# Kernel optimization log

Hardware: AMD Instinct MI355X
Metric: run time of the kernel (lower is better)

## Reference

```python
import jax, jax.numpy as jnp
import numpy as np

N_BLOCKS = 16
N_HEADS = 2
HEAD_DIM = 32
SCALE = HEAD_DIM ** (-0.5)


def setup_inputs() -> dict:
    key = jax.random.key(0)
    ks = jax.random.split(key, 5)
    b, s, d = 16, 4096, 1024
    nb, bd = N_BLOCKS, 1024 // N_BLOCKS  # block_dim = 64; emb per-block dim = 64
    w_std = 1.0 / np.sqrt(bd)
    inp = {
        'x': jax.random.normal(ks[0], (b, s, d), dtype=jnp.float32),
        'wq': jax.random.normal(ks[1], (nb, bd, bd), dtype=jnp.float32) * w_std,
        'bq': jnp.zeros((nb, bd), dtype=jnp.float32),
        'wk': jax.random.normal(ks[2], (nb, bd, bd), dtype=jnp.float32) * w_std,
        'bk': jnp.zeros((nb, bd), dtype=jnp.float32),
        'wv': jax.random.normal(ks[3], (nb, bd, bd), dtype=jnp.float32) * w_std,
        'bv': jnp.zeros((nb, bd), dtype=jnp.float32),
        'wf': jax.random.normal(ks[4], (nb, bd, bd), dtype=jnp.float32) * w_std,
        'bf': jnp.zeros((nb, bd), dtype=jnp.float32),
    }
    return inp


def _group_linear(x, w, b):
    # x: [B, S, G*I] -> per-block linear -> [B, S, G*O]
    B, S, _ = x.shape
    G, I, O = w.shape
    xg = x.reshape(B, S, G, I)
    y = jnp.einsum('bsgi,gio->bsgo', xg, w) + b
    return y.reshape(B, S, G * O)


def reference(x, wq, bq, wk, bk, wv, bv, wf, bf):
    B, S, D = x.shape
    nb, nh, hd = N_BLOCKS, N_HEADS, HEAD_DIM
    # grouped QKV projections -> [B, S, nb, nh, hd] -> heads before blocks
    q = _group_linear(x, wq, bq).reshape(B, S, nb, nh, hd).transpose(0, 1, 3, 2, 4) * SCALE
    k = _group_linear(x, wk, bk).reshape(B, S, nb, nh, hd).transpose(0, 1, 3, 2, 4)
    v = _group_linear(x, wv, bv).reshape(B, S, nb, nh, hd).transpose(0, 1, 3, 2, 4)
    # attention across blocks: score [B, S, nh, nb, nb]
    score = jnp.einsum('bshgd,bshfd->bshgf', q, k)
    score = jax.nn.softmax(score, axis=-1)
    out = jnp.einsum('bshgf,bshfd->bshgd', score, v)
    # back to [B, S, nb, nh, hd] then flatten
    out = out.transpose(0, 1, 3, 2, 4).reshape(B, S, nb * nh * hd)
    out = _group_linear(out, wf, bf)
    return out.reshape(B, S, D)
```

## Files before the change

### kernel.cpp

```cpp
#include <hip/hip_runtime.h>
#include <hip/hip_bf16.h>
#include <stdint.h>


typedef __attribute__((ext_vector_type(8))) short bf16x8;
typedef __attribute__((ext_vector_type(4))) float f32x4;

#define NTOK   65536
#define DM     1024
#define TT     16
#define QSCALE 0.17677669529663687f
#define LOG2E  1.4426950408889634f

static __device__ __forceinline__ unsigned short f2bf(float f) {
  unsigned int u = __float_as_uint(f);
  u += 0x7fffu + ((u >> 16) & 1u);
  return (unsigned short)(u >> 16);
}

static __device__ __forceinline__ unsigned int pk2(float a, float b) {
  return (unsigned int)f2bf(a) | ((unsigned int)f2bf(b) << 16);
}

static __device__ __forceinline__ bf16x8 pack8(float4 a, float4 b) {
  bf16x8 r;
  r[0] = (short)f2bf(a.x); r[1] = (short)f2bf(a.y);
  r[2] = (short)f2bf(a.z); r[3] = (short)f2bf(a.w);
  r[4] = (short)f2bf(b.x); r[5] = (short)f2bf(b.y);
  r[6] = (short)f2bf(b.z); r[7] = (short)f2bf(b.w);
  return r;
}

union FragCast { uint4 u4; bf16x8 v; uint2 u2[2]; unsigned int u[4]; };

__global__ void build_wfrag(const float* __restrict__ wq, const float* __restrict__ wk,
                            const float* __restrict__ wv, const float* __restrict__ wf,
                            uint4* __restrict__ wfrag) {
  int tid = blockIdx.x * 256 + threadIdx.x;
  if (tid >= 4 * 16 * 2 * 4 * 64) return;
  int lane =  tid        & 63;
  int nf   = (tid >> 6)  & 3;
  int kk   = (tid >> 8)  & 1;
  int g    = (tid >> 9)  & 15;
  int mat  =  tid >> 13;
  const float* w = (mat == 0) ? wq : (mat == 1) ? wk : (mat == 2) ? wv : wf;
  float sc = (mat == 0) ? QSCALE : 1.0f;
  int o  = nf * 16 + (lane & 15);
  int kb = kk * 32 + 8 * (lane >> 4);
  unsigned int packed[4];
#pragma unroll
  for (int jj = 0; jj < 4; ++jj) {
    unsigned short lo = f2bf(w[(g * 64 + kb + 2 * jj    ) * 64 + o] * sc);
    unsigned short hi = f2bf(w[(g * 64 + kb + 2 * jj + 1) * 64 + o] * sc);
    packed[jj] = (unsigned int)lo | ((unsigned int)hi << 16);
  }
  uint4 u; u.x = packed[0]; u.y = packed[1]; u.z = packed[2]; u.w = packed[3];
  wfrag[tid] = u;
}

#define PH1(h_) do {                                                          \
  _Pragma("unroll")                                                           \
  for (int gi = 0; gi < 2; ++gi) {                                            \
    const int g = 2 * w + gi;                                                 \
    _Pragma("unroll")                                                         \
    for (int mat = 0; mat < 2; ++mat) {       \
      const float* bp = mat ? bk : bq;                                        \
      const float bsc = mat ? 1.0f : QSCALE;                                  \
      unsigned short* dst = mat ? s_k : s_q;                                  \
      _Pragma("unroll")                                                       \
      for (int nf2 = 0; nf2 < 2; ++nf2) {                                     \
        const int nf = 2 * (h_) + nf2;                                        \
        float4 b4 = *(const float4*)&bp[g * 64 + nf * 16 + 4 * lq];           \
        f32x4 a1 = {b4.x * bsc, b4.y * bsc, b4.z * bsc, b4.w * bsc};          \
        _Pragma("unroll")                                                     \
        for (int kk = 0; kk < 2; ++kk) {                                      \
          FragCast fc;                                                        \
          fc.u4 = wfrag[(((mat * 16 + g) * 2 + kk) * 4 + nf) * 64 + lane];    \
          a1 = __builtin_amdgcn_mfma_f32_16x16x32_bf16(fc.v, afr[gi][kk], a1, 0, 0, 0); \
        }                                                                     \
             \
        uint2 w2; w2.x = pk2(a1[0], a1[1]); w2.y = pk2(a1[2], a1[3]);         \
        const int blk = (16 * (2 * nf2 + (lq >> 1)) + g) ^ (lr & 7);          \
        *(uint2*)&dst[lr * 512 + blk * 8 + 4 * (lq & 1)] = w2;                \
      }                                                                       \
    }                                                                         \
    _Pragma("unroll")                                                         \
    for (int nf2 = 0; nf2 < 2; ++nf2) {         \
      const int nf = 2 * (h_) + nf2;                                          \
      const float bias = bv[g * 64 + nf * 16 + lr];                           \
      f32x4 a1 = {bias, bias, bias, bias};                                    \
      _Pragma("unroll")                                                       \
      for (int kk = 0; kk < 2; ++kk) {                                        \
        FragCast fc;                                                          \
        fc.u4 = wfrag[(((2 * 16 + g) * 2 + kk) * 4 + nf) * 64 + lane];        \
        a1 = __builtin_amdgcn_mfma_f32_16x16x32_bf16(afr[gi][kk], fc.v, a1, 0, 0, 0); \
      }                                                                       \
                   \
      const int L = 16 * (g >> 2) + lr;                                       \
      const int jj = g & 3;                                                   \
      _Pragma("unroll")                                                       \
      for (int r = 0; r < 4; ++r)                                             \
        s_v[((4 * lq + r) * 2 + nf2) * 256 + L * 4 + jj] = f2bf(a1[r]);       \
    }                                                                         \
  }                                                                           \
} while (0)

#define PH2() do {                                                            \
  _Pragma("unroll")                                                           \
  for (int tt = 0; tt < 2; ++tt) {                                            \
    const int t = 2 * w + tt;                                                 \
    f32x4 zero = {0.f, 0.f, 0.f, 0.f};                                        \
    FragCast qa, ka;                                                          \
    const int blk = lane ^ (t & 7);                                           \
    qa.u4 = *(const uint4*)&s_q[t * 512 + blk * 8];                           \
    ka.u4 = *(const uint4*)&s_k[t * 512 + blk * 8];                           \
                  \
    f32x4 sc4 = __builtin_amdgcn_mfma_f32_16x16x32_bf16(ka.v, qa.v, zero, 0, 0, 0); \
    float m = fmaxf(fmaxf(sc4[0], sc4[1]), fmaxf(sc4[2], sc4[3]));            \
    m = fmaxf(m, __shfl_xor(m, 16));                                          \
    m = fmaxf(m, __shfl_xor(m, 32));                                          \
    float p0 = exp2f((sc4[0] - m) * LOG2E);                                   \
    float p1 = exp2f((sc4[1] - m) * LOG2E);                                   \
    float p2 = exp2f((sc4[2] - m) * LOG2E);                                   \
    float p3 = exp2f((sc4[3] - m) * LOG2E);                                   \
    float s = p0 + p1 + p2 + p3;                                              \
    s += __shfl_xor(s, 16);                                                   \
    s += __shfl_xor(s, 32);                                                   \
    const float inv = __fdividef(1.0f, s);                                    \
    FragCast pa;                      \
    pa.u[0] = pk2(p0 * inv, p1 * inv);                                        \
    pa.u[1] = pk2(p2 * inv, p3 * inv);                                        \
    pa.u[2] = 0; pa.u[3] = 0;                                                 \
    _Pragma("unroll")                                                         \
    for (int nf = 0; nf < 2; ++nf) {                                          \
      FragCast va;              \
      va.u2[0] = *(const uint2*)&s_v[(t * 2 + nf) * 256 + lane * 4];          \
      va.u[2] = 0; va.u[3] = 0;                                               \
      f32x4 o4 = __builtin_amdgcn_mfma_f32_16x16x32_bf16(va.v, pa.v, zero, 0, 0, 0); \
                                   \
      uint2 w2; w2.x = pk2(o4[0], o4[1]); w2.y = pk2(o4[2], o4[3]);           \
      const int ablk = (16 * (2 * nf + (lq >> 1)) + lr) ^ (t & 7);            \
      *(uint2*)&s_att[t * 512 + ablk * 8 + 4 * (lq & 1)] = w2;                \
    }                                                                         \
  }                                                                           \
} while (0)

#define PH3(h_) do {                                                          \
  _Pragma("unroll")                                                           \
  for (int gi = 0; gi < 2; ++gi) {                                            \
    const int g = 2 * w + gi;                                                 \
    FragCast aa;                        \
    const int blk = (16 * lq + g) ^ (lr & 7);                                 \
    aa.u4 = *(const uint4*)&s_att[lr * 512 + blk * 8];                        \
    _Pragma("unroll")                                                         \
    for (int nf = 0; nf < 4; ++nf) {                                          \
      FragCast fc;                                                            \
      fc.u4 = wfrag[(((3 * 16 + g) * 2 + (h_)) * 4 + nf) * 64 + lane];        \
      acc[gi][nf] = __builtin_amdgcn_mfma_f32_16x16x32_bf16(fc.v, aa.v, acc[gi][nf], 0, 0, 0); \
    }                                                                         \
  }                                                                           \
} while (0)

__global__ __launch_bounds__(512, 4)
void fused_gc(const float* __restrict__ x,
              const float* __restrict__ bq, const float* __restrict__ bk,
              const float* __restrict__ bv, const float* __restrict__ bfb,
              const uint4* __restrict__ wfrag,
              float* __restrict__ out) {
  __shared__ __align__(16) unsigned short s_q  [16 * 512];
  __shared__ __align__(16) unsigned short s_k  [16 * 512];
  __shared__ __align__(16) unsigned short s_att[16 * 512];
  __shared__ __align__(16) unsigned short s_v  [16 * 2 * 64 * 4];

  const int tid  = threadIdx.x;
  const int w    = tid >> 6;
  const int lane = tid & 63;
  const int lr   = lane & 15;
  const int lq   = lane >> 4;
  const long tok0 = (long)blockIdx.x * TT;

  bf16x8 afr[2][2];
  {
    const float* xr = x + (tok0 + lr) * DM;
#pragma unroll
    for (int gi = 0; gi < 2; ++gi) {
      const int g = 2 * w + gi;
#pragma unroll
      for (int kk = 0; kk < 2; ++kk) {
        const float* p = xr + g * 64 + kk * 32 + 8 * lq;
        afr[gi][kk] = pack8(*(const float4*)p, *(const float4*)(p + 4));
      }
    }
  }

  f32x4 acc[2][4];

  PH1(0);
  __syncthreads();
  PH2();
  __syncthreads();

#pragma unroll
  for (int gi = 0; gi < 2; ++gi) {
    const int g = 2 * w + gi;
#pragma unroll
    for (int nf = 0; nf < 4; ++nf) {
      float4 b4 = *(const float4*)&bfb[g * 64 + nf * 16 + 4 * lq];
      acc[gi][nf][0] = b4.x; acc[gi][nf][1] = b4.y;
      acc[gi][nf][2] = b4.z; acc[gi][nf][3] = b4.w;
    }
  }
  PH3(0);
  PH1(1);
  __syncthreads();
  PH2();
  __syncthreads();
  PH3(1);

#pragma unroll
  for (int gi = 0; gi < 2; ++gi) {
    const int g = 2 * w + gi;
#pragma unroll
    for (int nf = 0; nf < 4; ++nf) {
      float4 o4;
      o4.x = acc[gi][nf][0]; o4.y = acc[gi][nf][1];
      o4.z = acc[gi][nf][2]; o4.w = acc[gi][nf][3];
      *(float4*)&out[(tok0 + lr) * DM + g * 64 + nf * 16 + 4 * lq] = o4;
    }
  }
}

extern "C" void kernel_launch(void* const* d_in, const int* in_sizes, int n_in,
                              void* d_out, int out_size, void* d_ws, size_t ws_size,
                              hipStream_t stream) {
  const float* x   = (const float*)d_in[0];
  const float* wq  = (const float*)d_in[1];
  const float* bq_ = (const float*)d_in[2];
  const float* wk  = (const float*)d_in[3];
  const float* bk_ = (const float*)d_in[4];
  const float* wv  = (const float*)d_in[5];
  const float* bv_ = (const float*)d_in[6];
  const float* wf  = (const float*)d_in[7];
  const float* bf_ = (const float*)d_in[8];
  (void)in_sizes; (void)n_in; (void)out_size; (void)ws_size;

  uint4* wfrag = (uint4*)d_ws;

  build_wfrag<<<128, 256, 0, stream>>>(wq, wk, wv, wf, wfrag);
  fused_gc<<<NTOK / TT, 512, 0, stream>>>(x, bq_, bk_, bv_, bf_, wfrag,
                                          (float*)d_out);
}
```

Before: 234.7 us.

## Batch-prefetch weight fragments ahead of MFMAs and use LDS-only barriers

Loads all Q/K/V weight fragments for each half into registers up front, and prefetches the output-projection fragments before the barriers so global loads overlap the PH2 attention phase. Replaces __syncthreads with a barrier that waits only on LDS counters, so in-flight global loads are not drained at each sync. It also swaps the manual bf16 rounding for the HIP intrinsic. This raises register pressure (24+8 extra uint4 fragments), which at launch bounds of 512 threads and 4 blocks may cause spills.

```diff
diff --git a/kernel.cpp b/kernel.cpp
--- a/kernel.cpp
+++ b/kernel.cpp
@@ -12,10 +12,15 @@
 #define QSCALE 0.17677669529663687f
 #define LOG2E  1.4426950408889634f
 
+#define WG_BARRIER() do {                                   \
+  asm volatile("s_waitcnt lgkmcnt(0)" ::: "memory");        \
+  __builtin_amdgcn_s_barrier();                             \
+} while (0)
+
 static __device__ __forceinline__ unsigned short f2bf(float f) {
-  unsigned int u = __float_as_uint(f);
-  u += 0x7fffu + ((u >> 16) & 1u);
-  return (unsigned short)(u >> 16);
+  union { __hip_bfloat16 h; unsigned short s; } cv;
+  cv.h = __float2bfloat16(f);
+  return cv.s;
 }
 
 static __device__ __forceinline__ unsigned int pk2(float a, float b) {
@@ -59,14 +64,30 @@
 }
 
 #define PH1(h_) do {                                                          \
+  FragCast fq[8], fk[8], fv[8];                                               \
   _Pragma("unroll")                                                           \
   for (int gi = 0; gi < 2; ++gi) {                                            \
     const int g = 2 * w + gi;                                                 \
     _Pragma("unroll")                                                         \
-    for (int mat = 0; mat < 2; ++mat) {       \
-      const float* bp = mat ? bk : bq;                                        \
-      const float bsc = mat ? 1.0f : QSCALE;                                  \
-      unsigned short* dst = mat ? s_k : s_q;                                  \
+    for (int kk = 0; kk < 2; ++kk) {                                          \
+      _Pragma("unroll")                                                       \
+      for (int nf2 = 0; nf2 < 2; ++nf2) {                                     \
+        const int nf = 2 * (h_) + nf2;                                        \
+        const int ix = gi * 4 + kk * 2 + nf2;                                 \
+        fq[ix].u4 = wfrag[(((0 * 16 + g) * 2 + kk) * 4 + nf) * 64 + lane];    \
+        fk[ix].u4 = wfrag[(((1 * 16 + g) * 2 + kk) * 4 + nf) * 64 + lane];    \
+        fv[ix].u4 = wfrag[(((2 * 16 + g) * 2 + kk) * 4 + nf) * 64 + lane];    \
+      }                                                                       \
+    }                                                                         \
+  }                                                                           \
+  _Pragma("unroll")                                                           \
+  for (int mat = 0; mat < 2; ++mat) {         \
+    const float* bp = mat ? bk : bq;                                          \
+    const float bsc = mat ? 1.0f : QSCALE;                                    \
+    unsigned short* dst = mat ? s_k : s_q;                                    \
+    _Pragma("unroll")                                                         \
+    for (int gi = 0; gi < 2; ++gi) {                                          \
+      const int g = 2 * w + gi;                                               \
       _Pragma("unroll")                                                       \
       for (int nf2 = 0; nf2 < 2; ++nf2) {                                     \
         const int nf = 2 * (h_) + nf2;                                        \
@@ -74,9 +95,9 @@
         f32x4 a1 = {b4.x * bsc, b4.y * bsc, b4.z * bsc, b4.w * bsc};          \
         _Pragma("unroll")                                                     \
         for (int kk = 0; kk < 2; ++kk) {                                      \
-          FragCast fc;                                                        \
-          fc.u4 = wfrag[(((mat * 16 + g) * 2 + kk) * 4 + nf) * 64 + lane];    \
-          a1 = __builtin_amdgcn_mfma_f32_16x16x32_bf16(fc.v, afr[gi][kk], a1, 0, 0, 0); \
+          a1 = __builtin_amdgcn_mfma_f32_16x16x32_bf16(                       \
+              (mat ? fk : fq)[gi * 4 + kk * 2 + nf2].v, afr[gi][kk], a1,      \
+              0, 0, 0);                                                       \
         }                                                                     \
              \
         uint2 w2; w2.x = pk2(a1[0], a1[1]); w2.y = pk2(a1[2], a1[3]);         \
@@ -84,16 +105,19 @@
         *(uint2*)&dst[lr * 512 + blk * 8 + 4 * (lq & 1)] = w2;                \
       }                                                                       \
     }                                                                         \
-    _Pragma("unroll")                                                         \
-    for (int nf2 = 0; nf2 < 2; ++nf2) {         \
+  }                                                                           \
+  _Pragma("unroll")                                                           \
+  for (int gi = 0; gi < 2; ++gi) {              \
+    const int g = 2 * w + gi;                                                 \
+    _Pragma("unroll")                                                         \
+    for (int nf2 = 0; nf2 < 2; ++nf2) {                                       \
       const int nf = 2 * (h_) + nf2;                                          \
       const float bias = bv[g * 64 + nf * 16 + lr];                           \
       f32x4 a1 = {bias, bias, bias, bias};                                    \
       _Pragma("unroll")                                                       \
       for (int kk = 0; kk < 2; ++kk) {                                        \
-        FragCast fc;                                                          \
-        fc.u4 = wfrag[(((2 * 16 + g) * 2 + kk) * 4 + nf) * 64 + lane];        \
-        a1 = __builtin_amdgcn_mfma_f32_16x16x32_bf16(afr[gi][kk], fc.v, a1, 0, 0, 0); \
+        a1 = __builtin_amdgcn_mfma_f32_16x16x32_bf16(                         \
+            afr[gi][kk], fv[gi * 4 + kk * 2 + nf2].v, a1, 0, 0, 0);           \
       }                                                                       \
                    \
       const int L = 16 * (g >> 2) + lr;                                       \
@@ -102,6 +126,16 @@
       for (int r = 0; r < 4; ++r)                                             \
         s_v[((4 * lq + r) * 2 + nf2) * 256 + L * 4 + jj] = f2bf(a1[r]);       \
     }                                                                         \
+  }                                                                           \
+} while (0)
+
+#define LOADF(h_) do {                                                        \
+  _Pragma("unroll")                                                           \
+  for (int gi = 0; gi < 2; ++gi) {                                            \
+    const int g = 2 * w + gi;                                                 \
+    _Pragma("unroll")                                                         \
+    for (int nf = 0; nf < 4; ++nf)                                            \
+      ff[gi * 4 + nf].u4 = wfrag[(((3 * 16 + g) * 2 + (h_)) * 4 + nf) * 64 + lane]; \
   }                                                                           \
 } while (0)
 
@@ -145,7 +179,7 @@
   }                                                                           \
 } while (0)
 
-#define PH3(h_) do {                                                          \
+#define PH3() do {                                                            \
   _Pragma("unroll")                                                           \
   for (int gi = 0; gi < 2; ++gi) {                                            \
     const int g = 2 * w + gi;                                                 \
@@ -154,9 +188,8 @@
     aa.u4 = *(const uint4*)&s_att[lr * 512 + blk * 8];                        \
     _Pragma("unroll")                                                         \
     for (int nf = 0; nf < 4; ++nf) {                                          \
-      FragCast fc;                                                            \
-      fc.u4 = wfrag[(((3 * 16 + g) * 2 + (h_)) * 4 + nf) * 64 + lane];        \
-      acc[gi][nf] = __builtin_amdgcn_mfma_f32_16x16x32_bf16(fc.v, aa.v, acc[gi][nf], 0, 0, 0); \
+      acc[gi][nf] = __builtin_amdgcn_mfma_f32_16x16x32_bf16(                  \
+          ff[gi * 4 + nf].v, aa.v, acc[gi][nf], 0, 0, 0);                     \
     }                                                                         \
   }                                                                           \
 } while (0)
@@ -194,12 +227,10 @@
   }
 
   f32x4 acc[2][4];
+  FragCast ff[8];
 
   PH1(0);
-  __syncthreads();
-  PH2();
-  __syncthreads();
-
+  LOADF(0);
 #pragma unroll
   for (int gi = 0; gi < 2; ++gi) {
     const int g = 2 * w + gi;
@@ -210,12 +241,16 @@
       acc[gi][nf][2] = b4.z; acc[gi][nf][3] = b4.w;
     }
   }
-  PH3(0);
+  WG_BARRIER();
+  PH2();
+  WG_BARRIER();
+  PH3();
   PH1(1);
-  __syncthreads();
+  LOADF(1);
+  WG_BARRIER();
   PH2();
-  __syncthreads();
-  PH3(1);
+  WG_BARRIER();
+  PH3();
 
 #pragma unroll
   for (int gi = 0; gi < 2; ++gi) {
```

Result: slower. 334.7 us (+42.6%).

## Split final grouped projection into separate kernel via global attention buffer

Applied to the files above, without the earlier changes.

When the workspace is large enough, the fused kernel stops after attention and writes bf16 attention outputs to a global buffer in MFMA fragment layout. A second kernel then runs the final grouped linear from that buffer. This frees the s_att shared memory and the output accumulators in the first kernel, which may raise occupancy, at the cost of an extra 128MB global round trip. It also swaps the manual bf16 rounding for the library conversion and hoists weight fragment loads in the QKV phase.

```diff
diff --git a/kernel.cpp b/kernel.cpp
--- a/kernel.cpp
+++ b/kernel.cpp
@@ -13,9 +13,9 @@
 #define LOG2E  1.4426950408889634f
 
 static __device__ __forceinline__ unsigned short f2bf(float f) {
-  unsigned int u = __float_as_uint(f);
-  u += 0x7fffu + ((u >> 16) & 1u);
-  return (unsigned short)(u >> 16);
+  union { __hip_bfloat16 h; unsigned short s; } cv;
+  cv.h = __float2bfloat16(f);
+  return cv.s;
 }
 
 static __device__ __forceinline__ unsigned int pk2(float a, float b) {
@@ -37,7 +37,7 @@
                             const float* __restrict__ wv, const float* __restrict__ wf,
                             uint4* __restrict__ wfrag) {
   int tid = blockIdx.x * 256 + threadIdx.x;
-  if (tid >= 4 * 16 * 2 * 4 * 64) return;
+  if (tid >= 5 * 16 * 2 * 4 * 64) return;
   int lane =  tid        & 63;
   int nf   = (tid >> 6)  & 3;
   int kk   = (tid >> 8)  & 1;
@@ -45,67 +45,94 @@
   int mat  =  tid >> 13;
   const float* w = (mat == 0) ? wq : (mat == 1) ? wk : (mat == 2) ? wv : wf;
   float sc = (mat == 0) ? QSCALE : 1.0f;
-  int o  = nf * 16 + (lane & 15);
-  int kb = kk * 32 + 8 * (lane >> 4);
+  int o = nf * 16 + (lane & 15);
   unsigned int packed[4];
-#pragma unroll
-  for (int jj = 0; jj < 4; ++jj) {
-    unsigned short lo = f2bf(w[(g * 64 + kb + 2 * jj    ) * 64 + o] * sc);
-    unsigned short hi = f2bf(w[(g * 64 + kb + 2 * jj + 1) * 64 + o] * sc);
-    packed[jj] = (unsigned int)lo | ((unsigned int)hi << 16);
+  if (mat == 4) {
+#pragma unroll
+    for (int jj = 0; jj < 4; ++jj) {
+      int d0 = kk * 32 + ((jj >> 1) ? 16 : 0) + 4 * (lane >> 4) + 2 * (jj & 1);
+      unsigned short lo = f2bf(w[(g * 64 + d0    ) * 64 + o]);
+      unsigned short hi = f2bf(w[(g * 64 + d0 + 1) * 64 + o]);
+      packed[jj] = (unsigned int)lo | ((unsigned int)hi << 16);
+    }
+  } else {
+    int kb = kk * 32 + 8 * (lane >> 4);
+#pragma unroll
+    for (int jj = 0; jj < 4; ++jj) {
+      unsigned short lo = f2bf(w[(g * 64 + kb + 2 * jj    ) * 64 + o] * sc);
+      unsigned short hi = f2bf(w[(g * 64 + kb + 2 * jj + 1) * 64 + o] * sc);
+      packed[jj] = (unsigned int)lo | ((unsigned int)hi << 16);
+    }
   }
   uint4 u; u.x = packed[0]; u.y = packed[1]; u.z = packed[2]; u.w = packed[3];
   wfrag[tid] = u;
 }
 
-#define PH1(h_) do {                                                          \
+#define QK_ONE(g_, gi_, nf2_, h_, fwa_, fwb_, bp_, bsc_, dst_) do {           \
+  const int nf = 2 * (h_) + (nf2_);                                           \
+  float4 b4 = *(const float4*)&(bp_)[(g_) * 64 + nf * 16 + 4 * lq];           \
+  f32x4 a1 = {b4.x * (bsc_), b4.y * (bsc_), b4.z * (bsc_), b4.w * (bsc_)};    \
+  a1 = __builtin_amdgcn_mfma_f32_16x16x32_bf16((fwa_).v, afr[gi_][0], a1, 0, 0, 0); \
+  a1 = __builtin_amdgcn_mfma_f32_16x16x32_bf16((fwb_).v, afr[gi_][1], a1, 0, 0, 0); \
+          \
+  uint2 w2; w2.x = pk2(a1[0], a1[1]); w2.y = pk2(a1[2], a1[3]);               \
+  const int blk = (16 * (2 * (nf2_) + (lq >> 1)) + (g_)) ^ (lr & 7);          \
+  *(uint2*)&(dst_)[lr * 512 + blk * 8 + 4 * (lq & 1)] = w2;                   \
+} while (0)
+
+#define PH1_MAT(h_, mofs_, bp_, bsc_, dst_) do {                              \
   _Pragma("unroll")                                                           \
   for (int gi = 0; gi < 2; ++gi) {                                            \
     const int g = 2 * w + gi;                                                 \
-    _Pragma("unroll")                                                         \
-    for (int mat = 0; mat < 2; ++mat) {       \
-      const float* bp = mat ? bk : bq;                                        \
-      const float bsc = mat ? 1.0f : QSCALE;                                  \
-      unsigned short* dst = mat ? s_k : s_q;                                  \
-      _Pragma("unroll")                                                       \
-      for (int nf2 = 0; nf2 < 2; ++nf2) {                                     \
-        const int nf = 2 * (h_) + nf2;                                        \
-        float4 b4 = *(const float4*)&bp[g * 64 + nf * 16 + 4 * lq];           \
-        f32x4 a1 = {b4.x * bsc, b4.y * bsc, b4.z * bsc, b4.w * bsc};          \
-        _Pragma("unroll")                                                     \
-        for (int kk = 0; kk < 2; ++kk) {                                      \
-          FragCast fc;                                                        \
-          fc.u4 = wfrag[(((mat * 16 + g) * 2 + kk) * 4 + nf) * 64 + lane];    \
-          a1 = __builtin_amdgcn_mfma_f32_16x16x32_bf16(fc.v, afr[gi][kk], a1, 0, 0, 0); \
-        }                                                                     \
-             \
-        uint2 w2; w2.x = pk2(a1[0], a1[1]); w2.y = pk2(a1[2], a1[3]);         \
-        const int blk = (16 * (2 * nf2 + (lq >> 1)) + g) ^ (lr & 7);          \
-        *(uint2*)&dst[lr * 512 + blk * 8 + 4 * (lq & 1)] = w2;                \
-      }                                                                       \
-    }                                                                         \
-    _Pragma("unroll")                                                         \
-    for (int nf2 = 0; nf2 < 2; ++nf2) {         \
-      const int nf = 2 * (h_) + nf2;                                          \
-      const float bias = bv[g * 64 + nf * 16 + lr];                           \
+    FragCast f00, f01, f10, f11;                \
+    f00.u4 = wfrag[((((mofs_) + g) * 2 + 0) * 4 + 2 * (h_)    ) * 64 + lane]; \
+    f01.u4 = wfrag[((((mofs_) + g) * 2 + 0) * 4 + 2 * (h_) + 1) * 64 + lane]; \
+    f10.u4 = wfrag[((((mofs_) + g) * 2 + 1) * 4 + 2 * (h_)    ) * 64 + lane]; \
+    f11.u4 = wfrag[((((mofs_) + g) * 2 + 1) * 4 + 2 * (h_) + 1) * 64 + lane]; \
+    QK_ONE(g, gi, 0, h_, f00, f10, bp_, bsc_, dst_);                          \
+    QK_ONE(g, gi, 1, h_, f01, f11, bp_, bsc_, dst_);                          \
+  }                                                                           \
+} while (0)
+
+#define PH1_V(h_) do {                                                        \
+  _Pragma("unroll")                                                           \
+  for (int gi = 0; gi < 2; ++gi) {                                            \
+    const int g = 2 * w + gi;                                                 \
+    FragCast f00, f01, f10, f11;                                              \
+    f00.u4 = wfrag[(((2 * 16 + g) * 2 + 0) * 4 + 2 * (h_)    ) * 64 + lane];  \
+    f01.u4 = wfrag[(((2 * 16 + g) * 2 + 0) * 4 + 2 * (h_) + 1) * 64 + lane];  \
+    f10.u4 = wfrag[(((2 * 16 + g) * 2 + 1) * 4 + 2 * (h_)    ) * 64 + lane];  \
+    f11.u4 = wfrag[(((2 * 16 + g) * 2 + 1) * 4 + 2 * (h_) + 1) * 64 + lane];  \
+    const int L = 16 * (g >> 2) + lr;                                         \
+    const int jj = g & 3;                                                     \
+    {                                                                         \
+      const float bias = bv[g * 64 + (2 * (h_)) * 16 + lr];                   \
       f32x4 a1 = {bias, bias, bias, bias};                                    \
-      _Pragma("unroll")                                                       \
-      for (int kk = 0; kk < 2; ++kk) {                                        \
-        FragCast fc;                                                          \
-        fc.u4 = wfrag[(((2 * 16 + g) * 2 + kk) * 4 + nf) * 64 + lane];        \
-        a1 = __builtin_amdgcn_mfma_f32_16x16x32_bf16(afr[gi][kk], fc.v, a1, 0, 0, 0); \
-      }                                                                       \
-                   \
-      const int L = 16 * (g >> 2) + lr;                                       \
-      const int jj = g & 3;                                                   \
+      a1 = __builtin_amdgcn_mfma_f32_16x16x32_bf16(afr[gi][0], f00.v, a1, 0, 0, 0); \
+      a1 = __builtin_amdgcn_mfma_f32_16x16x32_bf16(afr[gi][1], f10.v, a1, 0, 0, 0); \
       _Pragma("unroll")                                                       \
       for (int r = 0; r < 4; ++r)                                             \
-        s_v[((4 * lq + r) * 2 + nf2) * 256 + L * 4 + jj] = f2bf(a1[r]);       \
+        s_v[((4 * lq + r) * 2 + 0) * 256 + L * 4 + jj] = f2bf(a1[r]);         \
+    }                                                                         \
+    {                                                                         \
+      const float bias = bv[g * 64 + (2 * (h_) + 1) * 16 + lr];               \
+      f32x4 a1 = {bias, bias, bias, bias};                                    \
+      a1 = __builtin_amdgcn_mfma_f32_16x16x32_bf16(afr[gi][0], f01.v, a1, 0, 0, 0); \
+      a1 = __builtin_amdgcn_mfma_f32_16x16x32_bf16(afr[gi][1], f11.v, a1, 0, 0, 0); \
+      _Pragma("unroll")                                                       \
+      for (int r = 0; r < 4; ++r)                                             \
+        s_v[((4 * lq + r) * 2 + 1) * 256 + L * 4 + jj] = f2bf(a1[r]);         \
     }                                                                         \
   }                                                                           \
 } while (0)
 
-#define PH2() do {                                                            \
+#define PH1(h_) do {                                                          \
+  PH1_MAT(h_, 0,  bq, QSCALE, s_q);                                           \
+  PH1_MAT(h_, 16, bk, 1.0f,   s_k);                                           \
+  PH1_V(h_);                                                                  \
+} while (0)
+
+#define PH2(h_) do {                                                          \
   _Pragma("unroll")                                                           \
   for (int tt = 0; tt < 2; ++tt) {                                            \
     const int t = 2 * w + tt;                                                 \
@@ -131,16 +158,27 @@
     pa.u[0] = pk2(p0 * inv, p1 * inv);                                        \
     pa.u[1] = pk2(p2 * inv, p3 * inv);                                        \
     pa.u[2] = 0; pa.u[3] = 0;                                                 \
-    _Pragma("unroll")                                                         \
-    for (int nf = 0; nf < 2; ++nf) {                                          \
-      FragCast va;              \
-      va.u2[0] = *(const uint2*)&s_v[(t * 2 + nf) * 256 + lane * 4];          \
-      va.u[2] = 0; va.u[3] = 0;                                               \
-      f32x4 o4 = __builtin_amdgcn_mfma_f32_16x16x32_bf16(va.v, pa.v, zero, 0, 0, 0); \
+    FragCast va0, va1;          \
+    va0.u2[0] = *(const uint2*)&s_v[(t * 2 + 0) * 256 + lane * 4];            \
+    va0.u[2] = 0; va0.u[3] = 0;                                               \
+    va1.u2[0] = *(const uint2*)&s_v[(t * 2 + 1) * 256 + lane * 4];            \
+    va1.u[2] = 0; va1.u[3] = 0;                                               \
                                    \
-      uint2 w2; w2.x = pk2(o4[0], o4[1]); w2.y = pk2(o4[2], o4[3]);           \
-      const int ablk = (16 * (2 * nf + (lq >> 1)) + lr) ^ (t & 7);            \
-      *(uint2*)&s_att[t * 512 + ablk * 8 + 4 * (lq & 1)] = w2;                \
+    f32x4 oo0 = __builtin_amdgcn_mfma_f32_16x16x32_bf16(va0.v, pa.v, zero, 0, 0, 0); \
+    f32x4 oo1 = __builtin_amdgcn_mfma_f32_16x16x32_bf16(va1.v, pa.v, zero, 0, 0, 0); \
+    if constexpr (SPLIT) {                                                    \
+      \
+      uint4 u;                                                                \
+      u.x = pk2(oo0[0], oo0[1]); u.y = pk2(oo0[2], oo0[3]);                   \
+      u.z = pk2(oo1[0], oo1[1]); u.w = pk2(oo1[2], oo1[3]);                   \
+      attw[((((int)blockIdx.x * 16 + lr) * 16 + t) * 2 + (h_)) * 4 + lq] = u; \
+    } else {                                                                  \
+      uint2 w20; w20.x = pk2(oo0[0], oo0[1]); w20.y = pk2(oo0[2], oo0[3]);    \
+      const int ab0 = (16 * (0 + (lq >> 1)) + lr) ^ (t & 7);                  \
+      *(uint2*)&s_att[t * 512 + ab0 * 8 + 4 * (lq & 1)] = w20;                \
+      uint2 w21; w21.x = pk2(oo1[0], oo1[1]); w21.y = pk2(oo1[2], oo1[3]);    \
+      const int ab1 = (16 * (2 + (lq >> 1)) + lr) ^ (t & 7);                  \
+      *(uint2*)&s_att[t * 512 + ab1 * 8 + 4 * (lq & 1)] = w21;                \
     }                                                                         \
   }                                                                           \
 } while (0)
@@ -161,16 +199,18 @@
   }                                                                           \
 } while (0)
 
+template <int SPLIT>
 __global__ __launch_bounds__(512, 4)
 void fused_gc(const float* __restrict__ x,
               const float* __restrict__ bq, const float* __restrict__ bk,
               const float* __restrict__ bv, const float* __restrict__ bfb,
               const uint4* __restrict__ wfrag,
+              uint4* __restrict__ attw,
               float* __restrict__ out) {
   __shared__ __align__(16) unsigned short s_q  [16 * 512];
   __shared__ __align__(16) unsigned short s_k  [16 * 512];
-  __shared__ __align__(16) unsigned short s_att[16 * 512];
   __shared__ __align__(16) unsigned short s_v  [16 * 2 * 64 * 4];
+  __shared__ __align__(16) unsigned short s_att[SPLIT ? 16 : 16 * 512];
 
   const int tid  = threadIdx.x;
   const int w    = tid >> 6;
@@ -193,38 +233,76 @@
     }
   }
 
-  f32x4 acc[2][4];
-
-  PH1(0);
-  __syncthreads();
-  PH2();
-  __syncthreads();
+  if constexpr (SPLIT) {
+    PH1(0);
+    __syncthreads();
+    PH2(0);
+    __syncthreads();
+    PH1(1);
+    __syncthreads();
+    PH2(1);
+  } else {
+    f32x4 acc[2][4];
+    PH1(0);
+    __syncthreads();
+    PH2(0);
+    __syncthreads();
+#pragma unroll
+    for (int gi = 0; gi < 2; ++gi) {
+      const int g = 2 * w + gi;
+#pragma unroll
+      for (int nf = 0; nf < 4; ++nf) {
+        float4 b4 = *(const float4*)&bfb[g * 64 + nf * 16 + 4 * lq];
+        acc[gi][nf][0] = b4.x; acc[gi][nf][1] = b4.y;
+        acc[gi][nf][2] = b4.z; acc[gi][nf][3] = b4.w;
+      }
+    }
+    PH3(0);
+    PH1(1);
+    __syncthreads();
+    PH2(1);
+    __syncthreads();
+    PH3(1);
+#pragma unroll
+    for (int gi = 0; gi < 2; ++gi) {
+      const int g = 2 * w + gi;
+#pragma unroll
+      for (int nf = 0; nf < 4; ++nf) {
+        float4 o4;
+        o4.x = acc[gi][nf][0]; o4.y = acc[gi][nf][1];
+        o4.z = acc[gi][nf][2]; o4.w = acc[gi][nf][3];
+        *(float4*)&out[(tok0 + lr) * DM + g * 64 + nf * 16 + 4 * lq] = o4;
+      }
+    }
+  }
+}
+
+__global__ __launch_bounds__(512, 2)
+void final_gemm(const float* __restrict__ bfb, const uint4* __restrict__ wfrag,
+                const uint4* __restrict__ attw, float* __restrict__ out) {
+  const int tid  = threadIdx.x;
+  const int w    = tid >> 6;
+  const int lane = tid & 63;
+  const int lr   = lane & 15;
+  const int lq   = lane >> 4;
+  const long tok0 = (long)blockIdx.x * TT;
 
 #pragma unroll
   for (int gi = 0; gi < 2; ++gi) {
     const int g = 2 * w + gi;
+    FragCast fb0, fb1;
+    fb0.u4 = attw[((((int)blockIdx.x * 16 + g) * 16 + lr) * 2 + 0) * 4 + lq];
+    fb1.u4 = attw[((((int)blockIdx.x * 16 + g) * 16 + lr) * 2 + 1) * 4 + lq];
 #pragma unroll
     for (int nf = 0; nf < 4; ++nf) {
       float4 b4 = *(const float4*)&bfb[g * 64 + nf * 16 + 4 * lq];
-      acc[gi][nf][0] = b4.x; acc[gi][nf][1] = b4.y;
-      acc[gi][nf][2] = b4.z; acc[gi][nf][3] = b4.w;
-    }
-  }
-  PH3(0);
-  PH1(1);
-  __syncthreads();
-  PH2();
-  __syncthreads();
-  PH3(1);
-
-#pragma unroll
-  for (int gi = 0; gi < 2; ++gi) {
-    const int g = 2 * w + gi;
-#pragma unroll
-    for (int nf = 0; nf < 4; ++nf) {
-      float4 o4;
-      o4.x = acc[gi][nf][0]; o4.y = acc[gi][nf][1];
-      o4.z = acc[gi][nf][2]; o4.w = acc[gi][nf][3];
+      f32x4 a1 = {b4.x, b4.y, b4.z, b4.w};
+      FragCast fa0, fa1;
+      fa0.u4 = wfrag[(((4 * 16 + g) * 2 + 0) * 4 + nf) * 64 + lane];
+      fa1.u4 = wfrag[(((4 * 16 + g) * 2 + 1) * 4 + nf) * 64 + lane];
+      a1 = __builtin_amdgcn_mfma_f32_16x16x32_bf16(fa0.v, fb0.v, a1, 0, 0, 0);
+      a1 = __builtin_amdgcn_mfma_f32_16x16x32_bf16(fa1.v, fb1.v, a1, 0, 0, 0);
+      float4 o4; o4.x = a1[0]; o4.y = a1[1]; o4.z = a1[2]; o4.w = a1[3];
       *(float4*)&out[(tok0 + lr) * DM + g * 64 + nf * 16 + 4 * lq] = o4;
     }
   }
@@ -242,11 +320,20 @@
   const float* bv_ = (const float*)d_in[6];
   const float* wf  = (const float*)d_in[7];
   const float* bf_ = (const float*)d_in[8];
-  (void)in_sizes; (void)n_in; (void)out_size; (void)ws_size;
+  (void)in_sizes; (void)n_in; (void)out_size;
 
   uint4* wfrag = (uint4*)d_ws;
-
-  build_wfrag<<<128, 256, 0, stream>>>(wq, wk, wv, wf, wfrag);
-  fused_gc<<<NTOK / TT, 512, 0, stream>>>(x, bq_, bk_, bv_, bf_, wfrag,
-                                          (float*)d_out);
-}
+  uint4* attw  = (uint4*)((char*)d_ws + (1u << 20));
+  const size_t need = (1u << 20) + (size_t)128 * 1024 * 1024;
+  const bool split = (ws_size >= need);
+
+  build_wfrag<<<160, 256, 0, stream>>>(wq, wk, wv, wf, wfrag);
+  if (split) {
+    fused_gc<1><<<NTOK / TT, 512, 0, stream>>>(x, bq_, bk_, bv_, bf_, wfrag,
+                                               attw, (float*)d_out);
+    final_gemm<<<NTOK / TT, 512, 0, stream>>>(bf_, wfrag, attw, (float*)d_out);
+  } else {
+    fused_gc<0><<<NTOK / TT, 512, 0, stream>>>(x, bq_, bk_, bv_, bf_, wfrag,
+                                               attw, (float*)d_out);
+  }
+}
```

New measurement: 292.0 us. +24.4%, slower.

## Use one wave per block group with 1024-thread workgroups

Applied to the files above, without the earlier changes.

The fused kernel now launches 1024 threads per workgroup with one wave per feature group instead of each wave handling two groups, halving per-thread work and register use. Weight fragments are hoisted into explicit loads ahead of the MFMAs, and bf16 conversion switches to the library intrinsic. This aims for more wave-level parallelism and latency hiding, at the cost of larger workgroups, more barrier participants and a stricter occupancy bound from launch_bounds(1024,8).

```diff
diff --git a/kernel.cpp b/kernel.cpp
--- a/kernel.cpp
+++ b/kernel.cpp
@@ -13,9 +13,9 @@
 #define LOG2E  1.4426950408889634f
 
 static __device__ __forceinline__ unsigned short f2bf(float f) {
-  unsigned int u = __float_as_uint(f);
-  u += 0x7fffu + ((u >> 16) & 1u);
-  return (unsigned short)(u >> 16);
+  union { __hip_bfloat16 h; unsigned short s; } cv;
+  cv.h = __float2bfloat16(f);
+  return cv.s;
 }
 
 static __device__ __forceinline__ unsigned int pk2(float a, float b) {
@@ -58,157 +58,156 @@
   wfrag[tid] = u;
 }
 
+
+#define QK_ONE(fA_, fB_, nf2_, h_, bp_, bsc_, dst_) do {                      \
+  const int nf = 2 * (h_) + (nf2_);                                           \
+  float4 b4 = *(const float4*)&(bp_)[g * 64 + nf * 16 + 4 * lq];              \
+  f32x4 a1 = {b4.x * (bsc_), b4.y * (bsc_), b4.z * (bsc_), b4.w * (bsc_)};    \
+  a1 = __builtin_amdgcn_mfma_f32_16x16x32_bf16((fA_).v, afr0, a1, 0, 0, 0);   \
+  a1 = __builtin_amdgcn_mfma_f32_16x16x32_bf16((fB_).v, afr1, a1, 0, 0, 0);   \
+  uint2 w2; w2.x = pk2(a1[0], a1[1]); w2.y = pk2(a1[2], a1[3]);               \
+  const int blk = (16 * (2 * (nf2_) + (lq >> 1)) + g) ^ (lr & 7);             \
+  *(uint2*)&(dst_)[lr * 512 + blk * 8 + 4 * (lq & 1)] = w2;                   \
+} while (0)
+
+#define V_ONE(fA_, fB_, nf2_, h_) do {                                        \
+  const int nf = 2 * (h_) + (nf2_);                                           \
+  const float bias = bv[g * 64 + nf * 16 + lr];                               \
+  f32x4 a1 = {bias, bias, bias, bias};                                        \
+  a1 = __builtin_amdgcn_mfma_f32_16x16x32_bf16(afr0, (fA_).v, a1, 0, 0, 0);   \
+  a1 = __builtin_amdgcn_mfma_f32_16x16x32_bf16(afr1, (fB_).v, a1, 0, 0, 0);   \
+  const int L = 16 * (g >> 2) + lr;                                           \
+  const int jj = g & 3;                                                       \
+  _Pragma("unroll")                                                           \
+  for (int r = 0; r < 4; ++r)                                                 \
+    s_v[((4 * lq + r) * 2 + (nf2_)) * 256 + L * 4 + jj] = f2bf(a1[r]);        \
+} while (0)
+
 #define PH1(h_) do {                                                          \
-  _Pragma("unroll")                                                           \
-  for (int gi = 0; gi < 2; ++gi) {                                            \
-    const int g = 2 * w + gi;                                                 \
-    _Pragma("unroll")                                                         \
-    for (int mat = 0; mat < 2; ++mat) {       \
-      const float* bp = mat ? bk : bq;                                        \
-      const float bsc = mat ? 1.0f : QSCALE;                                  \
-      unsigned short* dst = mat ? s_k : s_q;                                  \
-      _Pragma("unroll")                                                       \
-      for (int nf2 = 0; nf2 < 2; ++nf2) {                                     \
-        const int nf = 2 * (h_) + nf2;                                        \
-        float4 b4 = *(const float4*)&bp[g * 64 + nf * 16 + 4 * lq];           \
-        f32x4 a1 = {b4.x * bsc, b4.y * bsc, b4.z * bsc, b4.w * bsc};          \
-        _Pragma("unroll")                                                     \
-        for (int kk = 0; kk < 2; ++kk) {                                      \
-          FragCast fc;                                                        \
-          fc.u4 = wfrag[(((mat * 16 + g) * 2 + kk) * 4 + nf) * 64 + lane];    \
-          a1 = __builtin_amdgcn_mfma_f32_16x16x32_bf16(fc.v, afr[gi][kk], a1, 0, 0, 0); \
-        }                                                                     \
-             \
-        uint2 w2; w2.x = pk2(a1[0], a1[1]); w2.y = pk2(a1[2], a1[3]);         \
-        const int blk = (16 * (2 * nf2 + (lq >> 1)) + g) ^ (lr & 7);          \
-        *(uint2*)&dst[lr * 512 + blk * 8 + 4 * (lq & 1)] = w2;                \
-      }                                                                       \
-    }                                                                         \
-    _Pragma("unroll")                                                         \
-    for (int nf2 = 0; nf2 < 2; ++nf2) {         \
-      const int nf = 2 * (h_) + nf2;                                          \
-      const float bias = bv[g * 64 + nf * 16 + lr];                           \
-      f32x4 a1 = {bias, bias, bias, bias};                                    \
-      _Pragma("unroll")                                                       \
-      for (int kk = 0; kk < 2; ++kk) {                                        \
-        FragCast fc;                                                          \
-        fc.u4 = wfrag[(((2 * 16 + g) * 2 + kk) * 4 + nf) * 64 + lane];        \
-        a1 = __builtin_amdgcn_mfma_f32_16x16x32_bf16(afr[gi][kk], fc.v, a1, 0, 0, 0); \
-      }                                                                       \
-                   \
-      const int L = 16 * (g >> 2) + lr;                                       \
-      const int jj = g & 3;                                                   \
-      _Pragma("unroll")                                                       \
-      for (int r = 0; r < 4; ++r)                                             \
-        s_v[((4 * lq + r) * 2 + nf2) * 256 + L * 4 + jj] = f2bf(a1[r]);       \
-    }                                                                         \
+  {                                                                           \
+    FragCast qa0, qb0, qa1, qb1;                            \
+    qa0.u4 = wfrag[(((0 * 16 + g) * 2 + 0) * 4 + 2 * (h_)    ) * 64 + lane];  \
+    qb0.u4 = wfrag[(((0 * 16 + g) * 2 + 0) * 4 + 2 * (h_) + 1) * 64 + lane];  \
+    qa1.u4 = wfrag[(((0 * 16 + g) * 2 + 1) * 4 + 2 * (h_)    ) * 64 + lane];  \
+    qb1.u4 = wfrag[(((0 * 16 + g) * 2 + 1) * 4 + 2 * (h_) + 1) * 64 + lane];  \
+    QK_ONE(qa0, qa1, 0, h_, bq, QSCALE, s_q);                                 \
+    QK_ONE(qb0, qb1, 1, h_, bq, QSCALE, s_q);                                 \
   }                                                                           \
+  {                                                                           \
+    FragCast ka0, kb0, ka1, kb1;                                              \
+    ka0.u4 = wfrag[(((1 * 16 + g) * 2 + 0) * 4 + 2 * (h_)    ) * 64 + lane];  \
+    kb0.u4 = wfrag[(((1 * 16 + g) * 2 + 0) * 4 + 2 * (h_) + 1) * 64 + lane];  \
+    ka1.u4 = wfrag[(((1 * 16 + g) * 2 + 1) * 4 + 2 * (h_)    ) * 64 + lane];  \
+    kb1.u4 = wfrag[(((1 * 16 + g) * 2 + 1) * 4 + 2 * (h_) + 1) * 64 + lane];  \
+    QK_ONE(ka0, ka1, 0, h_, bk, 1.0f, s_k);                                   \
+    QK_ONE(kb0, kb1, 1, h_, bk, 1.0f, s_k);                                   \
+  }                                                                           \
+  {                                                                           \
+    FragCast va0, vb0, va1, vb1;                                              \
+    va0.u4 = wfrag[(((2 * 16 + g) * 2 + 0) * 4 + 2 * (h_)    ) * 64 + lane];  \
+    vb0.u4 = wfrag[(((2 * 16 + g) * 2 + 0) * 4 + 2 * (h_) + 1) * 64 + lane];  \
+    va1.u4 = wfrag[(((2 * 16 + g) * 2 + 1) * 4 + 2 * (h_)    ) * 64 + lane];  \
+    vb1.u4 = wfrag[(((2 * 16 + g) * 2 + 1) * 4 + 2 * (h_) + 1) * 64 + lane];  \
+    V_ONE(va0, va1, 0, h_);                                                   \
+    V_ONE(vb0, vb1, 1, h_);                                                   \
+  }                                                                           \
 } while (0)
 
 #define PH2() do {                                                            \
-  _Pragma("unroll")                                                           \
-  for (int tt = 0; tt < 2; ++tt) {                                            \
-    const int t = 2 * w + tt;                                                 \
-    f32x4 zero = {0.f, 0.f, 0.f, 0.f};                                        \
-    FragCast qa, ka;                                                          \
-    const int blk = lane ^ (t & 7);                                           \
-    qa.u4 = *(const uint4*)&s_q[t * 512 + blk * 8];                           \
-    ka.u4 = *(const uint4*)&s_k[t * 512 + blk * 8];                           \
+  const int t = g;                                                            \
+  f32x4 zero = {0.f, 0.f, 0.f, 0.f};                                          \
+  FragCast qa, ka;                                                            \
+  const int blk = lane ^ (t & 7);                                             \
+  qa.u4 = *(const uint4*)&s_q[t * 512 + blk * 8];                             \
+  ka.u4 = *(const uint4*)&s_k[t * 512 + blk * 8];                             \
                   \
-    f32x4 sc4 = __builtin_amdgcn_mfma_f32_16x16x32_bf16(ka.v, qa.v, zero, 0, 0, 0); \
-    float m = fmaxf(fmaxf(sc4[0], sc4[1]), fmaxf(sc4[2], sc4[3]));            \
-    m = fmaxf(m, __shfl_xor(m, 16));                                          \
-    m = fmaxf(m, __shfl_xor(m, 32));                                          \
-    float p0 = exp2f((sc4[0] - m) * LOG2E);                                   \
-    float p1 = exp2f((sc4[1] - m) * LOG2E);                                   \
-    float p2 = exp2f((sc4[2] - m) * LOG2E);                                   \
-    float p3 = exp2f((sc4[3] - m) * LOG2E);                                   \
-    float s = p0 + p1 + p2 + p3;                                              \
-    s += __shfl_xor(s, 16);                                                   \
-    s += __shfl_xor(s, 32);                                                   \
-    const float inv = __fdividef(1.0f, s);                                    \
-    FragCast pa;                      \
-    pa.u[0] = pk2(p0 * inv, p1 * inv);                                        \
-    pa.u[1] = pk2(p2 * inv, p3 * inv);                                        \
-    pa.u[2] = 0; pa.u[3] = 0;                                                 \
-    _Pragma("unroll")                                                         \
-    for (int nf = 0; nf < 2; ++nf) {                                          \
-      FragCast va;              \
-      va.u2[0] = *(const uint2*)&s_v[(t * 2 + nf) * 256 + lane * 4];          \
-      va.u[2] = 0; va.u[3] = 0;                                               \
-      f32x4 o4 = __builtin_amdgcn_mfma_f32_16x16x32_bf16(va.v, pa.v, zero, 0, 0, 0); \
+  f32x4 sc4 = __builtin_amdgcn_mfma_f32_16x16x32_bf16(ka.v, qa.v, zero, 0, 0, 0); \
+  float m = fmaxf(fmaxf(sc4[0], sc4[1]), fmaxf(sc4[2], sc4[3]));              \
+  m = fmaxf(m, __shfl_xor(m, 16));                                            \
+  m = fmaxf(m, __shfl_xor(m, 32));                                            \
+  float p0 = exp2f((sc4[0] - m) * LOG2E);                                     \
+  float p1 = exp2f((sc4[1] - m) * LOG2E);                                     \
+  float p2 = exp2f((sc4[2] - m) * LOG2E);                                     \
+  float p3 = exp2f((sc4[3] - m) * LOG2E);                                     \
+  float s = p0 + p1 + p2 + p3;                                                \
+  s += __shfl_xor(s, 16);                                                     \
+  s += __shfl_xor(s, 32);                                                     \
+  const float inv = __fdividef(1.0f, s);                                      \
+  FragCast pa;                        \
+  pa.u[0] = pk2(p0 * inv, p1 * inv);                                          \
+  pa.u[1] = pk2(p2 * inv, p3 * inv);                                          \
+  pa.u[2] = 0; pa.u[3] = 0;                                                   \
+  FragCast va0, va1;            \
+  va0.u2[0] = *(const uint2*)&s_v[(t * 2 + 0) * 256 + lane * 4];              \
+  va0.u[2] = 0; va0.u[3] = 0;                                                 \
+  va1.u2[0] = *(const uint2*)&s_v[(t * 2 + 1) * 256 + lane * 4];              \
+  va1.u[2] = 0; va1.u[3] = 0;                                                 \
                                    \
-      uint2 w2; w2.x = pk2(o4[0], o4[1]); w2.y = pk2(o4[2], o4[3]);           \
-      const int ablk = (16 * (2 * nf + (lq >> 1)) + lr) ^ (t & 7);            \
-      *(uint2*)&s_att[t * 512 + ablk * 8 + 4 * (lq & 1)] = w2;                \
-    }                                                                         \
-  }                                                                           \
+  f32x4 oo0 = __builtin_amdgcn_mfma_f32_16x16x32_bf16(va0.v, pa.v, zero, 0, 0, 0); \
+  f32x4 oo1 = __builtin_amdgcn_mfma_f32_16x16x32_bf16(va1.v, pa.v, zero, 0, 0, 0); \
+  uint2 w20; w20.x = pk2(oo0[0], oo0[1]); w20.y = pk2(oo0[2], oo0[3]);        \
+  const int ab0 = (16 * (0 + (lq >> 1)) + lr) ^ (t & 7);                      \
+  *(uint2*)&s_att[t * 512 + ab0 * 8 + 4 * (lq & 1)] = w20;                    \
+  uint2 w21; w21.x = pk2(oo1[0], oo1[1]); w21.y = pk2(oo1[2], oo1[3]);        \
+  const int ab1 = (16 * (2 + (lq >> 1)) + lr) ^ (t & 7);                      \
+  *(uint2*)&s_att[t * 512 + ab1 * 8 + 4 * (lq & 1)] = w21;                    \
 } while (0)
 
 #define PH3(h_) do {                                                          \
-  _Pragma("unroll")                                                           \
-  for (int gi = 0; gi < 2; ++gi) {                                            \
-    const int g = 2 * w + gi;                                                 \
-    FragCast aa;                        \
-    const int blk = (16 * lq + g) ^ (lr & 7);                                 \
-    aa.u4 = *(const uint4*)&s_att[lr * 512 + blk * 8];                        \
-    _Pragma("unroll")                                                         \
-    for (int nf = 0; nf < 4; ++nf) {                                          \
-      FragCast fc;                                                            \
-      fc.u4 = wfrag[(((3 * 16 + g) * 2 + (h_)) * 4 + nf) * 64 + lane];        \
-      acc[gi][nf] = __builtin_amdgcn_mfma_f32_16x16x32_bf16(fc.v, aa.v, acc[gi][nf], 0, 0, 0); \
-    }                                                                         \
-  }                                                                           \
-} while (0)
-
-__global__ __launch_bounds__(512, 4)
-void fused_gc(const float* __restrict__ x,
-              const float* __restrict__ bq, const float* __restrict__ bk,
-              const float* __restrict__ bv, const float* __restrict__ bfb,
-              const uint4* __restrict__ wfrag,
-              float* __restrict__ out) {
+  FragCast f0, f1, f2, f3;                                                    \
+  f0.u4 = wfrag[(((3 * 16 + g) * 2 + (h_)) * 4 + 0) * 64 + lane];             \
+  f1.u4 = wfrag[(((3 * 16 + g) * 2 + (h_)) * 4 + 1) * 64 + lane];             \
+  f2.u4 = wfrag[(((3 * 16 + g) * 2 + (h_)) * 4 + 2) * 64 + lane];             \
+  f3.u4 = wfrag[(((3 * 16 + g) * 2 + (h_)) * 4 + 3) * 64 + lane];             \
+  const int blk3 = (16 * lq + g) ^ (lr & 7);                                  \
+  FragCast aa;                        \
+  aa.u4 = *(const uint4*)&s_att[lr * 512 + blk3 * 8];                         \
+  acc0 = __builtin_amdgcn_mfma_f32_16x16x32_bf16(f0.v, aa.v, acc0, 0, 0, 0);  \
+  acc1 = __builtin_amdgcn_mfma_f32_16x16x32_bf16(f1.v, aa.v, acc1, 0, 0, 0);  \
+  acc2 = __builtin_amdgcn_mfma_f32_16x16x32_bf16(f2.v, aa.v, acc2, 0, 0, 0);  \
+  acc3 = __builtin_amdgcn_mfma_f32_16x16x32_bf16(f3.v, aa.v, acc3, 0, 0, 0);  \
+} while (0)
+
+__global__ __launch_bounds__(1024, 8)
+void fused_gc16(const float* __restrict__ x,
+                const float* __restrict__ bq, const float* __restrict__ bk,
+                const float* __restrict__ bv, const float* __restrict__ bfb,
+                const uint4* __restrict__ wfrag,
+                float* __restrict__ out) {
   __shared__ __align__(16) unsigned short s_q  [16 * 512];
   __shared__ __align__(16) unsigned short s_k  [16 * 512];
+  __shared__ __align__(16) unsigned short s_v  [16 * 2 * 256];
   __shared__ __align__(16) unsigned short s_att[16 * 512];
-  __shared__ __align__(16) unsigned short s_v  [16 * 2 * 64 * 4];
 
   const int tid  = threadIdx.x;
-  const int w    = tid >> 6;
+  const int g    = tid >> 6;
   const int lane = tid & 63;
   const int lr   = lane & 15;
   const int lq   = lane >> 4;
   const long tok0 = (long)blockIdx.x * TT;
 
-  bf16x8 afr[2][2];
+  bf16x8 afr0, afr1;
   {
-    const float* xr = x + (tok0 + lr) * DM;
-#pragma unroll
-    for (int gi = 0; gi < 2; ++gi) {
-      const int g = 2 * w + gi;
-#pragma unroll
-      for (int kk = 0; kk < 2; ++kk) {
-        const float* p = xr + g * 64 + kk * 32 + 8 * lq;
-        afr[gi][kk] = pack8(*(const float4*)p, *(const float4*)(p + 4));
-      }
-    }
-  }
-
-  f32x4 acc[2][4];
+    const float* xr = x + (tok0 + lr) * DM + g * 64;
+    afr0 = pack8(*(const float4*)(xr + 8 * lq), *(const float4*)(xr + 8 * lq + 4));
+    afr1 = pack8(*(const float4*)(xr + 32 + 8 * lq), *(const float4*)(xr + 32 + 8 * lq + 4));
+  }
+
+  f32x4 acc0, acc1, acc2, acc3;
 
   PH1(0);
   __syncthreads();
   PH2();
   __syncthreads();
-
-#pragma unroll
-  for (int gi = 0; gi < 2; ++gi) {
-    const int g = 2 * w + gi;
-#pragma unroll
-    for (int nf = 0; nf < 4; ++nf) {
-      float4 b4 = *(const float4*)&bfb[g * 64 + nf * 16 + 4 * lq];
-      acc[gi][nf][0] = b4.x; acc[gi][nf][1] = b4.y;
-      acc[gi][nf][2] = b4.z; acc[gi][nf][3] = b4.w;
-    }
+  {
+    float4 b0 = *(const float4*)&bfb[g * 64 +  0 + 4 * lq];
+    float4 b1 = *(const float4*)&bfb[g * 64 + 16 + 4 * lq];
+    float4 b2 = *(const float4*)&bfb[g * 64 + 32 + 4 * lq];
+    float4 b3 = *(const float4*)&bfb[g * 64 + 48 + 4 * lq];
+    acc0[0] = b0.x; acc0[1] = b0.y; acc0[2] = b0.z; acc0[3] = b0.w;
+    acc1[0] = b1.x; acc1[1] = b1.y; acc1[2] = b1.z; acc1[3] = b1.w;
+    acc2[0] = b2.x; acc2[1] = b2.y; acc2[2] = b2.z; acc2[3] = b2.w;
+    acc3[0] = b3.x; acc3[1] = b3.y; acc3[2] = b3.z; acc3[3] = b3.w;
   }
   PH3(0);
   PH1(1);
@@ -217,16 +216,17 @@
   __syncthreads();
   PH3(1);
 
-#pragma unroll
-  for (int gi = 0; gi < 2; ++gi) {
-    const int g = 2 * w + gi;
-#pragma unroll
-    for (int nf = 0; nf < 4; ++nf) {
-      float4 o4;
-      o4.x = acc[gi][nf][0]; o4.y = acc[gi][nf][1];
-      o4.z = acc[gi][nf][2]; o4.w = acc[gi][nf][3];
-      *(float4*)&out[(tok0 + lr) * DM + g * 64 + nf * 16 + 4 * lq] = o4;
-    }
+  {
+    float* orow = out + (tok0 + lr) * DM + g * 64 + 4 * lq;
+    float4 o4;
+    o4.x = acc0[0]; o4.y = acc0[1]; o4.z = acc0[2]; o4.w = acc0[3];
+    *(float4*)(orow +  0) = o4;
+    o4.x = acc1[0]; o4.y = acc1[1]; o4.z = acc1[2]; o4.w = acc1[3];
+    *(float4*)(orow + 16) = o4;
+    o4.x = acc2[0]; o4.y = acc2[1]; o4.z = acc2[2]; o4.w = acc2[3];
+    *(float4*)(orow + 32) = o4;
+    o4.x = acc3[0]; o4.y = acc3[1]; o4.z = acc3[2]; o4.w = acc3[3];
+    *(float4*)(orow + 48) = o4;
   }
 }
 
@@ -247,6 +247,6 @@
   uint4* wfrag = (uint4*)d_ws;
 
   build_wfrag<<<128, 256, 0, stream>>>(wq, wk, wv, wf, wfrag);
-  fused_gc<<<NTOK / TT, 512, 0, stream>>>(x, bq_, bk_, bv_, bf_, wfrag,
-                                          (float*)d_out);
-}
+  fused_gc16<<<NTOK / TT, 1024, 0, stream>>>(x, bq_, bk_, bv_, bf_, wfrag,
+                                             (float*)d_out);
+}
```

Measured after the change: 238.8 us. About the same (+1.8%).
